# Optimization experiments

Hardware: AMD Instinct MI355X
Metric: run time of the kernel (lower is better)

The kernel has to match this reference:

```python
import jax, jax.numpy as jnp
import numpy as np

D_MODEL = 1024


def setup_inputs() -> dict:
    key = jax.random.key(0)
    ks = jax.random.split(key, 9)
    d = D_MODEL
    s = 1.0 / np.sqrt(d)
    return {
        "x": jax.random.normal(ks[0], (4, 2048, d), dtype=jnp.float32),
        "w_q": jax.random.normal(ks[1], (d, d), dtype=jnp.float32) * s,
        "b_q": jnp.zeros((d,), dtype=jnp.float32),
        "w_k": jax.random.normal(ks[2], (d, d), dtype=jnp.float32) * s,
        "b_k": jnp.zeros((d,), dtype=jnp.float32),
        "w_v": jax.random.normal(ks[3], (d, d), dtype=jnp.float32) * s,
        "b_v": jnp.zeros((d,), dtype=jnp.float32),
        "w_out": jax.random.normal(ks[4], (d, d), dtype=jnp.float32) * s,
        "b_out": jnp.zeros((d,), dtype=jnp.float32),
    }


def reference(x, w_q, b_q, w_k, b_k, w_v, b_v, w_out, b_out):
    d_model = x.shape[-1]
    # torch Linear: y = x @ W^T + b
    Q = jnp.einsum("bsd,ed->bse", x, w_q) + b_q
    K = jnp.einsum("bsd,ed->bse", x, w_k) + b_k
    V = jnp.einsum("bsd,ed->bse", x, w_v) + b_v
    scores = jnp.einsum("bqd,bkd->bqk", Q, K) / jnp.sqrt(jnp.float32(d_model)).astype(x.dtype)
    attn = jax.nn.softmax(scores, axis=-1)
    out = jnp.einsum("bqk,bkd->bqd", attn, V)
    return jnp.einsum("bsd,ed->bse", out, w_out) + b_out
```

## Files before the change

### kernel.cpp

```cpp
#include <hip/hip_runtime.h>


typedef __bf16 bf16x8 __attribute__((ext_vector_type(8)));
typedef float f32x4 __attribute__((ext_vector_type(4)));

__device__ __forceinline__ unsigned short f32_to_bf16(float f) {
  unsigned int u = __float_as_uint(f);
  u += 0x7fffu + ((u >> 16) & 1u);
  return (unsigned short)(u >> 16);
}

__device__ __forceinline__ void load_lds16(const void* g, void* l) {
  __builtin_amdgcn_global_load_lds(
      (const __attribute__((address_space(1))) void*)g,
      (__attribute__((address_space(3))) void*)l, 16, 0, 0);
}

__global__ __launch_bounds__(256) void cast_f32_bf16(
    const float4* __restrict__ in, ushort4* __restrict__ out, int n4) {
  int i = blockIdx.x * 256 + threadIdx.x;
  if (i < n4) {
    float4 f = in[i];
    ushort4 u;
    u.x = f32_to_bf16(f.x);
    u.y = f32_to_bf16(f.y);
    u.z = f32_to_bf16(f.z);
    u.w = f32_to_bf16(f.w);
    out[i] = u;
  }
}

__global__ __launch_bounds__(256) void concat3(
    const float* __restrict__ a, const float* __restrict__ b,
    const float* __restrict__ c, float* __restrict__ o) {
  int i = blockIdx.x * 256 + threadIdx.x;
  if (i < 1024)
    o[i] = a[i];
  else if (i < 2048)
    o[i] = b[i - 1024];
  else if (i < 3072)
    o[i] = c[i - 2048];
}

__global__ __launch_bounds__(512, 2) void gemm_bt128x256(
    const unsigned short* __restrict__ A, const unsigned short* __restrict__ B,
    void* __restrict__ C, const float* __restrict__ bias,
    int M, int N, int K, float alpha, int out_bf16, int lda, int ldb,
    long long sA, long long sB, long long sC) {
  __shared__ unsigned short As[3][128][64];
  __shared__ unsigned short Bs[3][256][64];

  const int bz = blockIdx.z;
  A += (long long)bz * sA;
  B += (long long)bz * sB;

  const int bm = blockIdx.y, bn = blockIdx.x;
  const int tid = threadIdx.x;
  const int lane = tid & 63, wave = tid >> 6;
  const int wr = wave >> 2;
  const int wc = wave & 3;
  const int l16 = lane & 15, quad = lane >> 4;
  const int pc0 = (quad ^ (l16 & 7)) * 8;
  const int pc1 = ((4 + quad) ^ (l16 & 7)) * 8;

  const int srow = tid >> 3;
  const int lch = (tid & 7) ^ (srow & 7);
  const unsigned short* gA0 = A + (long long)(bm * 128 + srow) * lda + lch * 8;
  const unsigned short* gB0 = B + (long long)(bn * 256 + srow) * ldb + lch * 8;

  f32x4 acc[4][4] = {};
  bf16x8 af[2][2];
  bf16x8 bf[4][2];

  const int NT = K >> 6;

#define STG_A(BUF, KT)                                                      \
  do {                                                                      \
    const unsigned short* _s = gA0 + (long long)(KT) * 64;                  \
    char* _d = (char*)&As[BUF][0][0] + wave * 1024;                         \
    load_lds16(_s, _d);                                                     \
    load_lds16(_s + (long long)64 * lda, _d + 8192);                        \
  } while (0)
#define STG_B(BUF, KT, J0, JN)                                              \
  do {                                                                      \
    const unsigned short* _s = gB0 + (long long)(KT) * 64;                  \
    char* _d = (char*)&Bs[BUF][0][0] + wave * 1024;                         \
    _Pragma("unroll") for (int _j = (J0); _j < (JN); ++_j)                  \
        load_lds16(_s + (long long)(_j * 64) * ldb, _d + _j * 8192);        \
  } while (0)

#define DSA(BUF, P)                                                         \
  do {                                                                      \
    _Pragma("unroll") for (int m2 = 0; m2 < 2; ++m2) {                      \
      const unsigned short* _r =                                            \
          &As[BUF][wr * 64 + ((P) * 2 + m2) * 16 + l16][0];                 \
      af[m2][0] = *(const bf16x8*)(_r + pc0);                               \
      af[m2][1] = *(const bf16x8*)(_r + pc1);                               \
    }                                                                       \
  } while (0)

#define DSB(BUF)                                                            \
  do {                                                                      \
    _Pragma("unroll") for (int ni = 0; ni < 4; ++ni) {                      \
      const unsigned short* _r = &Bs[BUF][wc * 64 + ni * 16 + l16][0];      \
      bf[ni][0] = *(const bf16x8*)(_r + pc0);                               \
      bf[ni][1] = *(const bf16x8*)(_r + pc1);                               \
    }                                                                       \
  } while (0)

#define MM(P)                                                               \
  do {                                                                      \
    _Pragma("unroll") for (int m2 = 0; m2 < 2; ++m2)                        \
        _Pragma("unroll") for (int ni = 0; ni < 4; ++ni) {                  \
      f32x4* _a = &acc[(P) * 2 + m2][ni];                                   \
      *_a = __builtin_amdgcn_mfma_f32_16x16x32_bf16(af[m2][0], bf[ni][0],   \
                                                    *_a, 0, 0, 0);          \
      *_a = __builtin_amdgcn_mfma_f32_16x16x32_bf16(af[m2][1], bf[ni][1],   \
                                                    *_a, 0, 0, 0);          \
    }                                                                       \
  } while (0)

#define BAR() __builtin_amdgcn_s_barrier()
#define WLG() asm volatile("s_waitcnt lgkmcnt(0)" ::: "memory")
#define WVM6() asm volatile("s_waitcnt vmcnt(6)" ::: "memory")
#define P1() __builtin_amdgcn_s_setprio(1)
#define P0() __builtin_amdgcn_s_setprio(0)

  STG_A(0, 0);
  STG_B(0, 0, 0, 4);
  STG_A(1, 1);
  STG_B(1, 1, 0, 4);
  WVM6();
  BAR();

  int cur = 0;
  for (int t = 0; t < NT; ++t) {
    int b2 = cur + 2;
    if (b2 >= 3) b2 -= 3;
    const int kt = (t + 2 < NT) ? t + 2 : NT - 1;
    DSB(cur);
    DSA(cur, 0);
    STG_A(b2, kt);
    STG_B(b2, kt, 0, 1);
    BAR();
    WLG();
    P1();
    MM(0);
    P0();
    BAR();
    DSA(cur, 1);
    STG_B(b2, kt, 1, 4);
    BAR();
    WLG();
    P1();
    MM(1);
    P0();
    WVM6();
    BAR();
    ++cur;
    if (cur == 3) cur = 0;
  }
  asm volatile("s_waitcnt vmcnt(0)" ::: "memory");

  const long long orow0 = (long long)bm * 128 + wr * 64 + quad * 4;
  const int ocol0 = bn * 256 + wc * 64 + l16;
  if (out_bf16) {
    unsigned short* Cp = (unsigned short*)C + (long long)bz * sC;
#pragma unroll
    for (int mi = 0; mi < 4; ++mi)
#pragma unroll
      for (int ni = 0; ni < 4; ++ni) {
        const int col = ocol0 + ni * 16;
        const float bv = bias ? bias[col] : 0.f;
#pragma unroll
        for (int r = 0; r < 4; ++r) {
          const float o = acc[mi][ni][r] * alpha + bv;
          Cp[(orow0 + mi * 16 + r) * N + col] = f32_to_bf16(o);
        }
      }
  } else {
    float* Cp = (float*)C + (long long)bz * sC;
#pragma unroll
    for (int mi = 0; mi < 4; ++mi)
#pragma unroll
      for (int ni = 0; ni < 4; ++ni) {
        const int col = ocol0 + ni * 16;
        const float bv = bias ? bias[col] : 0.f;
#pragma unroll
        for (int r = 0; r < 4; ++r) {
          const float o = acc[mi][ni][r] * alpha + bv;
          Cp[(orow0 + mi * 16 + r) * N + col] = o;
        }
      }
  }
#undef STG_A
#undef STG_B
#undef DSA
#undef DSB
#undef MM
#undef BAR
#undef WLG
#undef WVM6
#undef P1
#undef P0
}

__global__ __launch_bounds__(256) void transpose_v(
    const unsigned short* __restrict__ V, unsigned short* __restrict__ VT,
    int ldv) {
  __shared__ unsigned short tile[64][65];
  const int d0 = blockIdx.x * 64, s0 = blockIdx.y * 64, b = blockIdx.z;
  const int t = threadIdx.x;
  const unsigned short* src = V + ((long long)b * 2048 + s0) * ldv + d0;
#pragma unroll
  for (int i = 0; i < 16; i++) {
    int lin = t + i * 256;
    int r = lin >> 6, c = lin & 63;
    tile[r][c] = src[(long long)r * ldv + c];
  }
  __syncthreads();
  unsigned short* dst = VT + ((long long)b * 1024 + d0) * 2048 + s0;
#pragma unroll
  for (int i = 0; i < 16; i++) {
    int lin = t + i * 256;
    int r = lin >> 6, c = lin & 63;
    dst[(long long)r * 2048 + c] = tile[c][r];
  }
}

__global__ __launch_bounds__(256) void softmax_rows(
    const float* __restrict__ S, unsigned short* __restrict__ P) {
  const long long row = blockIdx.x;
  const float* s = S + row * 2048;
  const int t = threadIdx.x;
  float v[8];
  float mx = -3.4e38f;
#pragma unroll
  for (int i = 0; i < 8; i++) {
    v[i] = s[t + i * 256];
    mx = fmaxf(mx, v[i]);
  }
#pragma unroll
  for (int o = 32; o >= 1; o >>= 1) mx = fmaxf(mx, __shfl_xor(mx, o));
  __shared__ float red[4], red2[4];
  if ((t & 63) == 0) red[t >> 6] = mx;
  __syncthreads();
  mx = fmaxf(fmaxf(red[0], red[1]), fmaxf(red[2], red[3]));
  float sum = 0.f;
#pragma unroll
  for (int i = 0; i < 8; i++) {
    v[i] = __expf(v[i] - mx);
    sum += v[i];
  }
#pragma unroll
  for (int o = 32; o >= 1; o >>= 1) sum += __shfl_xor(sum, o);
  if ((t & 63) == 0) red2[t >> 6] = sum;
  __syncthreads();
  sum = red2[0] + red2[1] + red2[2] + red2[3];
  const float inv = 1.0f / sum;
  unsigned short* p = P + row * 2048;
#pragma unroll
  for (int i = 0; i < 8; i++) p[t + i * 256] = f32_to_bf16(v[i] * inv);
}

extern "C" void kernel_launch(void* const* d_in, const int* in_sizes, int n_in,
                              void* d_out, int out_size, void* d_ws,
                              size_t ws_size, hipStream_t stream) {
  const float* x = (const float*)d_in[0];
  const float* wq = (const float*)d_in[1];
  const float* bq = (const float*)d_in[2];
  const float* wk = (const float*)d_in[3];
  const float* bk = (const float*)d_in[4];
  const float* wv = (const float*)d_in[5];
  const float* bv = (const float*)d_in[6];
  const float* wo = (const float*)d_in[7];
  const float* bo = (const float*)d_in[8];
  float* out = (float*)d_out;
  char* ws = (char*)d_ws;
  const size_t MB = 1ull << 20;

  unsigned short* xb   = (unsigned short*)(ws + 0);
  unsigned short* wqkv = (unsigned short*)(ws + 16 * MB);
  unsigned short* wkb  = (unsigned short*)(ws + 18 * MB);
  unsigned short* wvb  = (unsigned short*)(ws + 20 * MB);
  unsigned short* wob  = (unsigned short*)(ws + 22 * MB);
  unsigned short* QKV  = (unsigned short*)(ws + 24 * MB);
  float*          S    = (float*)(ws + 72 * MB);
  float*          bqkv = (float*)(ws + 72 * MB);
  unsigned short* VT   = xb;
  unsigned short* P    = QKV;
  unsigned short* O    = (unsigned short*)(ws + 56 * MB);

  cast_f32_bf16<<<dim3(8192), dim3(256), 0, stream>>>((const float4*)x,
                                                      (ushort4*)xb, 2097152);
  cast_f32_bf16<<<dim3(1024), dim3(256), 0, stream>>>((const float4*)wq,
                                                      (ushort4*)wqkv, 262144);
  cast_f32_bf16<<<dim3(1024), dim3(256), 0, stream>>>((const float4*)wk,
                                                      (ushort4*)wkb, 262144);
  cast_f32_bf16<<<dim3(1024), dim3(256), 0, stream>>>((const float4*)wv,
                                                      (ushort4*)wvb, 262144);
  cast_f32_bf16<<<dim3(1024), dim3(256), 0, stream>>>((const float4*)wo,
                                                      (ushort4*)wob, 262144);
  concat3<<<dim3(12), dim3(256), 0, stream>>>(bq, bk, bv, bqkv);

  gemm_bt128x256<<<dim3(12, 64, 1), dim3(512), 0, stream>>>(
      xb, wqkv, QKV, bqkv, 8192, 3072, 1024, 1.f, 1, 1024, 1024, 0, 0, 0);

  transpose_v<<<dim3(16, 32, 4), dim3(256), 0, stream>>>(QKV + 2048, VT, 3072);

  gemm_bt128x256<<<dim3(8, 16, 4), dim3(512), 0, stream>>>(
      QKV, QKV + 1024, S, nullptr, 2048, 2048, 1024, 0.03125f, 0, 3072, 3072,
      2048ll * 3072, 2048ll * 3072, 2048ll * 2048);

  softmax_rows<<<dim3(8192), dim3(256), 0, stream>>>(S, P);

  gemm_bt128x256<<<dim3(4, 16, 4), dim3(512), 0, stream>>>(
      P, VT, O, nullptr, 2048, 1024, 2048, 1.f, 1, 2048, 2048, 2048ll * 2048,
      1024ll * 2048, 2048ll * 1024);

  gemm_bt128x256<<<dim3(4, 64, 1), dim3(512), 0, stream>>>(
      O, wob, out, bo, 8192, 1024, 1024, 1.f, 0, 1024, 1024, 0, 0, 0);
}
```

Measured before the change: 314.6 us.

## Add 256x256-tile GEMM with split A/B buffering for QKV and score GEMMs

```diff
diff --git a/kernel.cpp b/kernel.cpp
--- a/kernel.cpp
+++ b/kernel.cpp
@@ -42,6 +42,193 @@
     o[i] = c[i - 2048];
 }
 
+__global__ __launch_bounds__(512, 2) void gemm_bt256dp(
+    const unsigned short* __restrict__ A, const unsigned short* __restrict__ B,
+    void* __restrict__ C, const float* __restrict__ bias,
+    int M, int N, int K, float alpha, int out_bf16, int lda, int ldb,
+    long long sA, long long sB, long long sC) {
+  __shared__ unsigned short As[3][2][128 * 64];
+  __shared__ unsigned short Bs[2][2][128 * 64];
+
+  const int bz = blockIdx.z;
+  A += (long long)bz * sA;
+  B += (long long)bz * sB;
+
+  const int bm = blockIdx.y, bn = blockIdx.x;
+  const int tid = threadIdx.x;
+  const int lane = tid & 63, wave = tid >> 6;
+  const int wr = wave >> 2;
+  const int wc = wave & 3;
+  const int l16 = lane & 15, quad = lane >> 4;
+  const int wbh = wc >> 1;
+  const int wbr = (wc & 1) * 64 + l16;
+  const int pc0 = (quad ^ (l16 & 7)) * 8;
+  const int pc1 = ((4 + quad) ^ (l16 & 7)) * 8;
+
+  const int srow = tid >> 3;
+  const int lch = (tid & 7) ^ (srow & 7);
+  const unsigned short* gA0 = A + (long long)(bm * 256 + srow) * lda + lch * 8;
+  const unsigned short* gB0 = B + (long long)(bn * 256 + srow) * ldb + lch * 8;
+
+  f32x4 acc[8][4] = {};
+  bf16x8 af[2][2];
+  bf16x8 bf[4][2];
+
+  const int NT = K >> 6;
+
+#define STA(BUF, H, KT)                                                     \
+  do {                                                                      \
+    const unsigned short* _s =                                              \
+        gA0 + (long long)(H) * 128 * lda + (long long)(KT) * 64;            \
+    char* _d = (char*)&As[BUF][H][0] + wave * 1024;                         \
+    load_lds16(_s, _d);                                                     \
+    load_lds16(_s + (long long)64 * lda, _d + 8192);                        \
+  } while (0)
+#define STB(BUF, H, KT)                                                     \
+  do {                                                                      \
+    const unsigned short* _s =                                              \
+        gB0 + (long long)(H) * 128 * ldb + (long long)(KT) * 64;            \
+    char* _d = (char*)&Bs[BUF][H][0] + wave * 1024;                         \
+    load_lds16(_s, _d);                                                     \
+    load_lds16(_s + (long long)64 * ldb, _d + 8192);                        \
+  } while (0)
+
+#define DSAq(BUF, MIP)                                                      \
+  do {                                                                      \
+    _Pragma("unroll") for (int m2 = 0; m2 < 2; ++m2) {                      \
+      const unsigned short* _r =                                            \
+          &As[BUF][wr][(((MIP) * 2 + m2) * 16 + l16) * 64];                 \
+      af[m2][0] = *(const bf16x8*)(_r + pc0);                               \
+      af[m2][1] = *(const bf16x8*)(_r + pc1);                               \
+    }                                                                       \
+  } while (0)
+
+#define DSBq(BUF)                                                           \
+  do {                                                                      \
+    _Pragma("unroll") for (int ni = 0; ni < 4; ++ni) {                      \
+      const unsigned short* _r = &Bs[BUF][wbh][(wbr + ni * 16) * 64];       \
+      bf[ni][0] = *(const bf16x8*)(_r + pc0);                               \
+      bf[ni][1] = *(const bf16x8*)(_r + pc1);                               \
+    }                                                                       \
+  } while (0)
+
+#define MMq(MIP)                                                            \
+  do {                                                                      \
+    _Pragma("unroll") for (int m2 = 0; m2 < 2; ++m2)                        \
+        _Pragma("unroll") for (int ni = 0; ni < 4; ++ni) {                  \
+      f32x4* _a = &acc[(MIP) * 2 + m2][ni];                                 \
+      *_a = __builtin_amdgcn_mfma_f32_16x16x32_bf16(af[m2][0], bf[ni][0],   \
+                                                    *_a, 0, 0, 0);          \
+      *_a = __builtin_amdgcn_mfma_f32_16x16x32_bf16(af[m2][1], bf[ni][1],   \
+                                                    *_a, 0, 0, 0);          \
+    }                                                                       \
+  } while (0)
+
+#define BARx() __builtin_amdgcn_s_barrier()
+#define WLGx() asm volatile("s_waitcnt lgkmcnt(0)" ::: "memory")
+#define WVM8() asm volatile("s_waitcnt vmcnt(8)" ::: "memory")
+#define PR1() __builtin_amdgcn_s_setprio(1)
+#define PR0() __builtin_amdgcn_s_setprio(0)
+
+  STA(0, 0, 0);
+  STA(0, 1, 0);
+  STB(0, 0, 0);
+  STB(0, 1, 0);
+  STA(1, 0, 1);
+  STA(1, 1, 1);
+  STB(1, 0, 1);
+  STB(1, 1, 1);
+  WVM8();
+  BARx();
+
+  int a = 0;
+  for (int t = 0; t < NT; ++t) {
+    const int b = t & 1;
+    int a2 = a + 2;
+    if (a2 >= 3) a2 -= 3;
+    const int kt2 = (t + 2 < NT) ? t + 2 : NT - 1;
+    DSBq(b);
+    DSAq(a, 0);
+    STA(a2, 0, kt2);
+    BARx();
+    WLGx();
+    PR1();
+    MMq(0);
+    PR0();
+    BARx();
+    DSAq(a, 1);
+    STA(a2, 1, kt2);
+    BARx();
+    WLGx();
+    PR1();
+    MMq(1);
+    PR0();
+    BARx();
+    DSAq(a, 2);
+    STB(b, 0, kt2);
+    BARx();
+    WLGx();
+    PR1();
+    MMq(2);
+    PR0();
+    BARx();
+    DSAq(a, 3);
+    STB(b, 1, kt2);
+    BARx();
+    WLGx();
+    PR1();
+    MMq(3);
+    PR0();
+    WVM8();
+    BARx();
+    ++a;
+    if (a == 3) a = 0;
+  }
+  asm volatile("s_waitcnt vmcnt(0)" ::: "memory");
+
+  const long long orow0 = (long long)bm * 256 + wr * 128 + quad * 4;
+  const int ocol0 = bn * 256 + wc * 64 + l16;
+  if (out_bf16) {
+    unsigned short* Cp = (unsigned short*)C + (long long)bz * sC;
+#pragma unroll
+    for (int mi = 0; mi < 8; ++mi)
+#pragma unroll
+      for (int ni = 0; ni < 4; ++ni) {
+        const int col = ocol0 + ni * 16;
+        const float bv = bias ? bias[col] : 0.f;
+#pragma unroll
+        for (int r = 0; r < 4; ++r) {
+          const float o = acc[mi][ni][r] * alpha + bv;
+          Cp[(orow0 + mi * 16 + r) * N + col] = f32_to_bf16(o);
+        }
+      }
+  } else {
+    float* Cp = (float*)C + (long long)bz * sC;
+#pragma unroll
+    for (int mi = 0; mi < 8; ++mi)
+#pragma unroll
+      for (int ni = 0; ni < 4; ++ni) {
+        const int col = ocol0 + ni * 16;
+        const float bv = bias ? bias[col] : 0.f;
+#pragma unroll
+        for (int r = 0; r < 4; ++r) {
+          const float o = acc[mi][ni][r] * alpha + bv;
+          Cp[(orow0 + mi * 16 + r) * N + col] = o;
+        }
+      }
+  }
+#undef STA
+#undef STB
+#undef DSAq
+#undef DSBq
+#undef MMq
+#undef BARx
+#undef WLGx
+#undef WVM8
+#undef PR1
+#undef PR0
+}
+
 __global__ __launch_bounds__(512, 2) void gemm_bt128x256(
     const unsigned short* __restrict__ A, const unsigned short* __restrict__ B,
     void* __restrict__ C, const float* __restrict__ bias,
@@ -123,8 +310,8 @@
 #define BAR() __builtin_amdgcn_s_barrier()
 #define WLG() asm volatile("s_waitcnt lgkmcnt(0)" ::: "memory")
 #define WVM6() asm volatile("s_waitcnt vmcnt(6)" ::: "memory")
-#define P1() __builtin_amdgcn_s_setprio(1)
-#define P0() __builtin_amdgcn_s_setprio(0)
+#define P1x() __builtin_amdgcn_s_setprio(1)
+#define P0x() __builtin_amdgcn_s_setprio(0)
 
   STG_A(0, 0);
   STG_B(0, 0, 0, 4);
@@ -144,17 +331,17 @@
     STG_B(b2, kt, 0, 1);
     BAR();
     WLG();
-    P1();
+    P1x();
     MM(0);
-    P0();
+    P0x();
     BAR();
     DSA(cur, 1);
     STG_B(b2, kt, 1, 4);
     BAR();
     WLG();
-    P1();
+    P1x();
     MM(1);
-    P0();
+    P0x();
     WVM6();
     BAR();
     ++cur;
@@ -201,8 +388,8 @@
 #undef BAR
 #undef WLG
 #undef WVM6
-#undef P1
-#undef P0
+#undef P1x
+#undef P0x
 }
 
 __global__ __launch_bounds__(256) void transpose_v(
@@ -303,12 +490,12 @@
                                                       (ushort4*)wob, 262144);
   concat3<<<dim3(12), dim3(256), 0, stream>>>(bq, bk, bv, bqkv);
 
-  gemm_bt128x256<<<dim3(12, 64, 1), dim3(512), 0, stream>>>(
+  gemm_bt256dp<<<dim3(12, 32, 1), dim3(512), 0, stream>>>(
       xb, wqkv, QKV, bqkv, 8192, 3072, 1024, 1.f, 1, 1024, 1024, 0, 0, 0);
 
   transpose_v<<<dim3(16, 32, 4), dim3(256), 0, stream>>>(QKV + 2048, VT, 3072);
 
-  gemm_bt128x256<<<dim3(8, 16, 4), dim3(512), 0, stream>>>(
+  gemm_bt256dp<<<dim3(8, 8, 4), dim3(512), 0, stream>>>(
       QKV, QKV + 1024, S, nullptr, 2048, 2048, 1024, 0.03125f, 0, 3072, 3072,
       2048ll * 3072, 2048ll * 3072, 2048ll * 2048);
 
```

New measurement: 314.3 us. About the same (-0.1%).

## Compute V transposed directly via swapped GEMM and fuse cast kernels

Applied to the files above, without the earlier changes.

```diff
diff --git a/kernel.cpp b/kernel.cpp
--- a/kernel.cpp
+++ b/kernel.cpp
@@ -10,43 +10,56 @@
   return (unsigned short)(u >> 16);
 }
 
+__device__ __forceinline__ ushort4 cvt4(float4 f) {
+  ushort4 u;
+  u.x = f32_to_bf16(f.x);
+  u.y = f32_to_bf16(f.y);
+  u.z = f32_to_bf16(f.z);
+  u.w = f32_to_bf16(f.w);
+  return u;
+}
+
 __device__ __forceinline__ void load_lds16(const void* g, void* l) {
   __builtin_amdgcn_global_load_lds(
       (const __attribute__((address_space(1))) void*)g,
       (__attribute__((address_space(3))) void*)l, 16, 0, 0);
 }
 
-__global__ __launch_bounds__(256) void cast_f32_bf16(
-    const float4* __restrict__ in, ushort4* __restrict__ out, int n4) {
+__global__ __launch_bounds__(256) void prep(
+    const float4* __restrict__ x, const float4* __restrict__ wq,
+    const float4* __restrict__ wk, const float4* __restrict__ wv,
+    const float4* __restrict__ wo, const float4* __restrict__ bq,
+    const float4* __restrict__ bk, ushort4* __restrict__ xb,
+    ushort4* __restrict__ wqk, ushort4* __restrict__ wvb,
+    ushort4* __restrict__ wob, float4* __restrict__ bqk) {
+  const int NX = 2097152;
+  const int NW = 262144;
   int i = blockIdx.x * 256 + threadIdx.x;
-  if (i < n4) {
-    float4 f = in[i];
-    ushort4 u;
-    u.x = f32_to_bf16(f.x);
-    u.y = f32_to_bf16(f.y);
-    u.z = f32_to_bf16(f.z);
-    u.w = f32_to_bf16(f.w);
-    out[i] = u;
-  }
-}
-
-__global__ __launch_bounds__(256) void concat3(
-    const float* __restrict__ a, const float* __restrict__ b,
-    const float* __restrict__ c, float* __restrict__ o) {
-  int i = blockIdx.x * 256 + threadIdx.x;
-  if (i < 1024)
-    o[i] = a[i];
-  else if (i < 2048)
-    o[i] = b[i - 1024];
-  else if (i < 3072)
-    o[i] = c[i - 2048];
+  if (i < NX) {
+    xb[i] = cvt4(x[i]);
+  } else if (i < NX + NW) {
+    int j = i - NX;
+    wqk[j] = cvt4(wq[j]);
+  } else if (i < NX + 2 * NW) {
+    int j = i - NX - NW;
+    wqk[NW + j] = cvt4(wk[j]);
+  } else if (i < NX + 3 * NW) {
+    int j = i - NX - 2 * NW;
+    wvb[j] = cvt4(wv[j]);
+  } else if (i < NX + 4 * NW) {
+    int j = i - NX - 3 * NW;
+    wob[j] = cvt4(wo[j]);
+  } else if (i < NX + 4 * NW + 512) {
+    int j = i - NX - 4 * NW;
+    bqk[j] = (j < 256) ? bq[j] : bk[j - 256];
+  }
 }
 
 __global__ __launch_bounds__(512, 2) void gemm_bt128x256(
     const unsigned short* __restrict__ A, const unsigned short* __restrict__ B,
     void* __restrict__ C, const float* __restrict__ bias,
-    int M, int N, int K, float alpha, int out_bf16, int lda, int ldb,
-    long long sA, long long sB, long long sC) {
+    int M, int N, int K, float alpha, int out_bf16, int bias_row,
+    int lda, int ldb, long long sA, long long sB, long long sC) {
   __shared__ unsigned short As[3][128][64];
   __shared__ unsigned short Bs[3][256][64];
 
@@ -123,8 +136,8 @@
 #define BAR() __builtin_amdgcn_s_barrier()
 #define WLG() asm volatile("s_waitcnt lgkmcnt(0)" ::: "memory")
 #define WVM6() asm volatile("s_waitcnt vmcnt(6)" ::: "memory")
-#define P1() __builtin_amdgcn_s_setprio(1)
-#define P0() __builtin_amdgcn_s_setprio(0)
+#define P1x() __builtin_amdgcn_s_setprio(1)
+#define P0x() __builtin_amdgcn_s_setprio(0)
 
   STG_A(0, 0);
   STG_B(0, 0, 0, 4);
@@ -144,17 +157,17 @@
     STG_B(b2, kt, 0, 1);
     BAR();
     WLG();
-    P1();
+    P1x();
     MM(0);
-    P0();
+    P0x();
     BAR();
     DSA(cur, 1);
     STG_B(b2, kt, 1, 4);
     BAR();
     WLG();
-    P1();
+    P1x();
     MM(1);
-    P0();
+    P0x();
     WVM6();
     BAR();
     ++cur;
@@ -171,9 +184,11 @@
 #pragma unroll
       for (int ni = 0; ni < 4; ++ni) {
         const int col = ocol0 + ni * 16;
-        const float bv = bias ? bias[col] : 0.f;
+        const float bcol = (bias && !bias_row) ? bias[col] : 0.f;
 #pragma unroll
         for (int r = 0; r < 4; ++r) {
+          const float bv =
+              (bias && bias_row) ? bias[orow0 + mi * 16 + r] : bcol;
           const float o = acc[mi][ni][r] * alpha + bv;
           Cp[(orow0 + mi * 16 + r) * N + col] = f32_to_bf16(o);
         }
@@ -185,9 +200,11 @@
 #pragma unroll
       for (int ni = 0; ni < 4; ++ni) {
         const int col = ocol0 + ni * 16;
-        const float bv = bias ? bias[col] : 0.f;
+        const float bcol = (bias && !bias_row) ? bias[col] : 0.f;
 #pragma unroll
         for (int r = 0; r < 4; ++r) {
+          const float bv =
+              (bias && bias_row) ? bias[orow0 + mi * 16 + r] : bcol;
           const float o = acc[mi][ni][r] * alpha + bv;
           Cp[(orow0 + mi * 16 + r) * N + col] = o;
         }
@@ -201,31 +218,8 @@
 #undef BAR
 #undef WLG
 #undef WVM6
-#undef P1
-#undef P0
-}
-
-__global__ __launch_bounds__(256) void transpose_v(
-    const unsigned short* __restrict__ V, unsigned short* __restrict__ VT,
-    int ldv) {
-  __shared__ unsigned short tile[64][65];
-  const int d0 = blockIdx.x * 64, s0 = blockIdx.y * 64, b = blockIdx.z;
-  const int t = threadIdx.x;
-  const unsigned short* src = V + ((long long)b * 2048 + s0) * ldv + d0;
-#pragma unroll
-  for (int i = 0; i < 16; i++) {
-    int lin = t + i * 256;
-    int r = lin >> 6, c = lin & 63;
-    tile[r][c] = src[(long long)r * ldv + c];
-  }
-  __syncthreads();
-  unsigned short* dst = VT + ((long long)b * 1024 + d0) * 2048 + s0;
-#pragma unroll
-  for (int i = 0; i < 16; i++) {
-    int lin = t + i * 256;
-    int r = lin >> 6, c = lin & 63;
-    dst[(long long)r * 2048 + c] = tile[c][r];
-  }
+#undef P1x
+#undef P0x
 }
 
 __global__ __launch_bounds__(256) void softmax_rows(
@@ -279,45 +273,39 @@
   char* ws = (char*)d_ws;
   const size_t MB = 1ull << 20;
 
-  unsigned short* xb   = (unsigned short*)(ws + 0);
-  unsigned short* wqkv = (unsigned short*)(ws + 16 * MB);
-  unsigned short* wkb  = (unsigned short*)(ws + 18 * MB);
-  unsigned short* wvb  = (unsigned short*)(ws + 20 * MB);
-  unsigned short* wob  = (unsigned short*)(ws + 22 * MB);
-  unsigned short* QKV  = (unsigned short*)(ws + 24 * MB);
-  float*          S    = (float*)(ws + 72 * MB);
-  float*          bqkv = (float*)(ws + 72 * MB);
-  unsigned short* VT   = xb;
-  unsigned short* P    = QKV;
-  unsigned short* O    = (unsigned short*)(ws + 56 * MB);
-
-  cast_f32_bf16<<<dim3(8192), dim3(256), 0, stream>>>((const float4*)x,
-                                                      (ushort4*)xb, 2097152);
-  cast_f32_bf16<<<dim3(1024), dim3(256), 0, stream>>>((const float4*)wq,
-                                                      (ushort4*)wqkv, 262144);
-  cast_f32_bf16<<<dim3(1024), dim3(256), 0, stream>>>((const float4*)wk,
-                                                      (ushort4*)wkb, 262144);
-  cast_f32_bf16<<<dim3(1024), dim3(256), 0, stream>>>((const float4*)wv,
-                                                      (ushort4*)wvb, 262144);
-  cast_f32_bf16<<<dim3(1024), dim3(256), 0, stream>>>((const float4*)wo,
-                                                      (ushort4*)wob, 262144);
-  concat3<<<dim3(12), dim3(256), 0, stream>>>(bq, bk, bv, bqkv);
-
-  gemm_bt128x256<<<dim3(12, 64, 1), dim3(512), 0, stream>>>(
-      xb, wqkv, QKV, bqkv, 8192, 3072, 1024, 1.f, 1, 1024, 1024, 0, 0, 0);
-
-  transpose_v<<<dim3(16, 32, 4), dim3(256), 0, stream>>>(QKV + 2048, VT, 3072);
+  unsigned short* xb  = (unsigned short*)(ws + 0);
+  unsigned short* wqk = (unsigned short*)(ws + 16 * MB);
+  unsigned short* wvb = (unsigned short*)(ws + 20 * MB);
+  unsigned short* wob = (unsigned short*)(ws + 22 * MB);
+  unsigned short* QKm = (unsigned short*)(ws + 24 * MB);
+  unsigned short* VT  = (unsigned short*)(ws + 56 * MB);
+  float*          S   = (float*)(ws + 72 * MB);
+  float*          bqk = (float*)(ws + 72 * MB);
+  unsigned short* P   = QKm;
+  unsigned short* O   = xb;
+
+  prep<<<dim3(12290), dim3(256), 0, stream>>>(
+      (const float4*)x, (const float4*)wq, (const float4*)wk,
+      (const float4*)wv, (const float4*)wo, (const float4*)bq,
+      (const float4*)bk, (ushort4*)xb, (ushort4*)wqk, (ushort4*)wvb,
+      (ushort4*)wob, (float4*)bqk);
+
+  gemm_bt128x256<<<dim3(8, 64, 1), dim3(512), 0, stream>>>(
+      xb, wqk, QKm, bqk, 8192, 2048, 1024, 1.f, 1, 0, 1024, 1024, 0, 0, 0);
+
+  gemm_bt128x256<<<dim3(32, 8, 1), dim3(512), 0, stream>>>(
+      wvb, xb, VT, bv, 1024, 8192, 1024, 1.f, 1, 1, 1024, 1024, 0, 0, 0);
 
   gemm_bt128x256<<<dim3(8, 16, 4), dim3(512), 0, stream>>>(
-      QKV, QKV + 1024, S, nullptr, 2048, 2048, 1024, 0.03125f, 0, 3072, 3072,
-      2048ll * 3072, 2048ll * 3072, 2048ll * 2048);
+      QKm, QKm + 1024, S, nullptr, 2048, 2048, 1024, 0.03125f, 0, 0, 2048,
+      2048, 2048ll * 2048, 2048ll * 2048, 2048ll * 2048);
 
   softmax_rows<<<dim3(8192), dim3(256), 0, stream>>>(S, P);
 
   gemm_bt128x256<<<dim3(4, 16, 4), dim3(512), 0, stream>>>(
-      P, VT, O, nullptr, 2048, 1024, 2048, 1.f, 1, 2048, 2048, 2048ll * 2048,
-      1024ll * 2048, 2048ll * 1024);
+      P, VT, O, nullptr, 2048, 1024, 2048, 1.f, 1, 0, 2048, 8192,
+      2048ll * 2048, 2048ll, 2048ll * 1024);
 
   gemm_bt128x256<<<dim3(4, 64, 1), dim3(512), 0, stream>>>(
-      O, wob, out, bo, 8192, 1024, 1024, 1.f, 0, 1024, 1024, 0, 0, 0);
-}
+      O, wob, out, bo, 8192, 1024, 1024, 1.f, 0, 0, 1024, 1024, 0, 0, 0);
+}
```

Measured after the change: 322.1 us. +2.4%, slower.
